# Performance work log

Measured on AMD Instinct MI355X. Metric: run time of the kernel, lower is better.

## Reference

```python
import jax, jax.numpy as jnp
import numpy as np

B, C, N, D, H, NC = 128, 9, 2048, 192, 384, 18  # batch, in_chans, time, embed, mlp_hidden, classes


def setup_inputs() -> dict:
    key = jax.random.key(0)
    ks = jax.random.split(key, 18)
    rn = lambda k, sh, s=0.02: jax.random.normal(k, sh, dtype=jnp.float32) * s
    return {
        "x": jax.random.normal(ks[0], (B, C, N), dtype=jnp.float32),
        "conv_w": rn(ks[1], (D, C, 3)),
        "conv_b": jnp.zeros((D,), jnp.float32),
        "pos_embed": jnp.zeros((1, N, D), jnp.float32),
        "qkv_w": rn(ks[2], (3 * D, D)),
        "qkv_b": jnp.zeros((3 * D,), jnp.float32),
        "proj_w": rn(ks[3], (D, D)),
        "proj_b": jnp.zeros((D,), jnp.float32),
        "ln1_g": jnp.ones((D,), jnp.float32),
        "ln1_b": jnp.zeros((D,), jnp.float32),
        "mlp_w1": rn(ks[4], (H, D)),
        "mlp_b1": jnp.zeros((H,), jnp.float32),
        "mlp_w2": rn(ks[5], (D, H)),
        "mlp_b2": jnp.zeros((D,), jnp.float32),
        "ln2_g": jnp.ones((D,), jnp.float32),
        "ln2_b": jnp.zeros((D,), jnp.float32),
        "head_w": rn(ks[6], (NC, D)),
        "head_b": jnp.zeros((NC,), jnp.float32),
    }


def _ln(x, g, b, eps=1e-5):
    m = x.mean(-1, keepdims=True)
    v = ((x - m) ** 2).mean(-1, keepdims=True)
    return (x - m) * jax.lax.rsqrt(v + eps) * g + b


def reference(x, conv_w, conv_b, pos_embed, qkv_w, qkv_b, proj_w, proj_b,
              ln1_g, ln1_b, mlp_w1, mlp_b1, mlp_w2, mlp_b2, ln2_g, ln2_b,
              head_w, head_b):
    # patch embed: Conv1d(C->D, k=3, pad=1), then [B, N, D]
    h = jax.lax.conv_general_dilated(
        x, conv_w, window_strides=(1,), padding=[(1, 1)],
        dimension_numbers=("NCH", "OIH", "NCH")) + conv_b[None, :, None]
    h = jnp.transpose(h, (0, 2, 1)) + pos_embed  # [B, N, D]

    # linear (Performer-style) attention with ReLU feature maps
    hn = _ln(h, ln1_g, ln1_b)
    qkv = hn @ qkv_w.T + qkv_b  # [B, N, 3D]
    q, k, v = jnp.split(qkv, 3, axis=-1)
    q = jax.nn.relu(q)
    k = jax.nn.relu(k)
    kv = jnp.einsum("bnd,bne->bde", k, v)       # [B, D, D]
    num = jnp.einsum("bnd,bde->bne", q, kv)      # [B, N, D]
    # NOTE: original sums q over BOTH token and feature dims -> scalar per batch
    denom = q.sum(axis=(1, 2))[:, None, None]
    attn = num / (denom + 1e-6)
    h = h + attn @ proj_w.T + proj_b

    # MLP block (exact GELU, as torch nn.GELU default)
    hn2 = _ln(h, ln2_g, ln2_b)
    m = jax.nn.gelu(hn2 @ mlp_w1.T + mlp_b1, approximate=False)
    h = h + m @ mlp_w2.T + mlp_b2

    # head: AdaptiveAvgPool1d(1) over time, then Linear
    pooled = h.mean(axis=1)  # [B, D]
    return pooled @ head_w.T + head_b  # [B, NC]
```

## Files before the change

kernel.cpp:

```cpp
#include <hip/hip_runtime.h>
#include <cmath>

#define B_   128
#define C_   9
#define N_   2048
#define D_   192
#define H_   384
#define NC_  18

typedef unsigned short ushort_t;
typedef __attribute__((ext_vector_type(8))) __bf16 bf16x8;
typedef __attribute__((ext_vector_type(8))) short short8;
typedef __attribute__((ext_vector_type(16))) float f32x16;

__device__ __forceinline__ ushort_t f2bf(float x) {
    unsigned u = __float_as_uint(x);
    return (ushort_t)((u + 0x7fffu + ((u >> 16) & 1u)) >> 16);
}
__device__ __forceinline__ float bf2f(ushort_t h) {
    return __uint_as_float(((unsigned)h) << 16);
}
__device__ __forceinline__ bf16x8 ldfrag(const ushort_t* p) {
    short8 s = *(const short8*)p;
    return __builtin_bit_cast(bf16x8, s);
}

#define APAD 12480

__global__ __launch_bounds__(192) void conv_ln_k(
    const float* __restrict__ x, const float* __restrict__ w,
    const float* __restrict__ cb, const float* __restrict__ pos,
    const float* __restrict__ lng, const float* __restrict__ lnb,
    float* __restrict__ h, ushort_t* __restrict__ oh, ushort_t* __restrict__ ol)
{
    const int n0 = blockIdx.x * 64;
    const int b  = blockIdx.y;
    const int d  = threadIdx.x;

    __shared__ float xs[C_][66];
    __shared__ float tile[64][193];
    __shared__ float ps[64][3], pq[64][3];
    __shared__ float mm[64], rr[64];

    for (int e = threadIdx.x; e < C_ * 66; e += 192) {
        int c = e / 66, i = e % 66;
        int n = n0 - 1 + i;
        xs[c][i] = (n >= 0 && n < N_) ? x[((size_t)b * C_ + c) * N_ + n] : 0.f;
    }
    float wr[C_][3];
#pragma unroll
    for (int c = 0; c < C_; ++c)
#pragma unroll
        for (int t = 0; t < 3; ++t) wr[c][t] = w[(d * C_ + c) * 3 + t];
    const float bias = cb[d];
    __syncthreads();

    for (int i = 0; i < 64; ++i) {
        float acc = bias + pos[(size_t)(n0 + i) * D_ + d];
#pragma unroll
        for (int c = 0; c < C_; ++c)
#pragma unroll
            for (int t = 0; t < 3; ++t) acc += xs[c][i + t] * wr[c][t];
        tile[i][d] = acc;
    }
    __syncthreads();

    {
        int row = threadIdx.x & 63, part = threadIdx.x >> 6;
        float s = 0.f, q = 0.f;
        const float* tr = &tile[row][part * 64];
#pragma unroll 8
        for (int j = 0; j < 64; ++j) { float v = tr[j]; s += v; q += v * v; }
        ps[row][part] = s; pq[row][part] = q;
    }
    __syncthreads();
    if (threadIdx.x < 64) {
        int r = threadIdx.x;
        float s = ps[r][0] + ps[r][1] + ps[r][2];
        float q = pq[r][0] + pq[r][1] + pq[r][2];
        float m = s * (1.f / D_);
        mm[r] = m;
        rr[r] = rsqrtf(q * (1.f / D_) - m * m + 1e-5f);
    }
    __syncthreads();
    {
        const float gd = lng[d], bd = lnb[d];
        for (int i = 0; i < 64; ++i) {
            float v = tile[i][d];
            size_t idx = ((size_t)b * N_ + n0 + i) * D_ + d;
            h[idx] = v;
            float nv = (v - mm[i]) * rr[i] * gd + bd;
            ushort_t hb = f2bf(nv);
            oh[idx] = hb;
            ol[idx] = f2bf(nv - bf2f(hb));
        }
    }
}

__global__ __launch_bounds__(256) void splitw_pack_k(
    const float* __restrict__ w, ushort_t* __restrict__ hi, ushort_t* __restrict__ lo,
    int NW, int K)
{
    int i = blockIdx.x * 256 + threadIdx.x;
    if (i >= NW * K) return;
    int row = i / K, k = i % K;
    int g = row / 192, c = row % 192;
    float v = w[i];
    ushort_t hb = f2bf(v);
    size_t o = (size_t)g * K * 192 + (size_t)(k >> 4) * 3072 + (size_t)c * 16 + (k & 15);
    hi[o] = hb;
    lo[o] = f2bf(v - bf2f(hb));
}

template <int EPI, int KT, int NBY>
__global__ __launch_bounds__(256) void mgemm(
    const ushort_t* __restrict__ Ah, const ushort_t* __restrict__ Al,
    const ushort_t* __restrict__ Wh, const ushort_t* __restrict__ Wl,
    const float* __restrict__ bias, float* __restrict__ dsum,
    const float* __restrict__ lng, const float* __restrict__ lnb,
    ushort_t* __restrict__ oh, ushort_t* __restrict__ ol,
    ushort_t* __restrict__ kTh, ushort_t* __restrict__ kTl,
    ushort_t* __restrict__ vTh, ushort_t* __restrict__ vTl,
    float* __restrict__ facc)
{
    extern __shared__ ushort_t smem[];
    constexpr int NS  = KT / 16;
    constexpr int APL = 12288;

    const int tid  = threadIdx.x;
    const int lane = tid & 63;
    const int l5   = lane >> 5;
    const int wid  = tid >> 6;
    const int wr = wid >> 1, wc = wid & 1;

    int bx, by;
    {
        int gmx = gridDim.x / NBY;
        int xx = blockIdx.x & 7, ii = blockIdx.x >> 3;
        by = ii % NBY;
        bx = xx * (gmx >> 3) + ii / NBY;
    }
    const int m0 = bx * 64;
    const int batch = m0 >> 11;

    size_t wbase = 0;
    if (EPI == 0) wbase = (size_t)by * 192 * KT;
    else if (EPI == 3) wbase = (size_t)batch * D_ * D_;
    const ushort_t* Whp = Wh + wbase;
    const ushort_t* Wlp = Wl + wbase;

    auto stageChunk = [&](int kr) {
#pragma unroll
        for (int i = 0; i < 12; ++i) {
            int c = wid + i * 4;
            int plane = c & 1, k8 = c >> 1;
            const ushort_t* ap = plane ? Al : Ah;
            const ushort_t* src = ap + (size_t)(m0 + lane) * KT + kr * 192 + k8 * 8;
            __builtin_amdgcn_global_load_lds(
                (const __attribute__((address_space(1))) void*)src,
                (__attribute__((address_space(3))) void*)(smem + plane * APL + k8 * 512),
                16, 0, 0);
        }
    };

    const int wcol = (wc * 96 + (lane & 31)) * 16 + l5 * 8;
    auto loadW = [&](int sg, bf16x8* w) {
#pragma unroll
        for (int tn = 0; tn < 3; ++tn) {
            size_t off = (size_t)sg * 3072 + wcol + tn * 512;
            w[tn * 2 + 0] = ldfrag(Whp + off);
            w[tn * 2 + 1] = ldfrag(Wlp + off);
        }
    };

    f32x16 acc[3] = {};
    const int arow = (wr * 32 + (lane & 31)) * 8;

    bf16x8 w0[6], w1[6], w2[6];
    loadW(0, w0);
    if (NS > 1) loadW(1, w1);
    if (NS > 2) loadW(2, w2);

#pragma unroll
    for (int s = 0; s < NS; ++s) {
        if ((s % 12) == 0) {
            if (s) __syncthreads();
            stageChunk(s / 12);
            __syncthreads();
        }
        bf16x8* wcur = (s % 3 == 0) ? w0 : ((s % 3 == 1) ? w1 : w2);
        int ao = ((s % 12) * 2 + l5) * 512 + arow;
        bf16x8 ah = ldfrag(smem + ao);
        bf16x8 al = ldfrag(smem + APL + ao);
#pragma unroll
        for (int tn = 0; tn < 3; ++tn) {
            acc[tn] = __builtin_amdgcn_mfma_f32_32x32x16_bf16(ah, wcur[tn * 2 + 0], acc[tn], 0, 0, 0);
            acc[tn] = __builtin_amdgcn_mfma_f32_32x32x16_bf16(ah, wcur[tn * 2 + 1], acc[tn], 0, 0, 0);
            acc[tn] = __builtin_amdgcn_mfma_f32_32x32x16_bf16(al, wcur[tn * 2 + 0], acc[tn], 0, 0, 0);
        }
        if (s + 3 < NS) loadW(s + 3, wcur);
    }

    const int cb = wc * 96 + (lane & 31);
    const int rb0 = m0 + wr * 32 + 4 * l5;
    const int rl0 = wr * 32 + 4 * l5;

    if (EPI == 0) {
        if (by == 0) {
            float qsum = 0.f;
            __syncthreads();
#pragma unroll
            for (int tn = 0; tn < 3; ++tn) {
                const int col = cb + tn * 32;
                const float bv = bias[col];
#pragma unroll
                for (int r = 0; r < 16; ++r) {
                    int rowl = rl0 + (r & 3) + 8 * (r >> 2);
                    float v = fmaxf(acc[tn][r] + bv, 0.f);
                    qsum += v;
                    ushort_t hb = f2bf(v);
                    smem[rowl * 192 + col] = hb;
                    smem[APL + rowl * 192 + col] = f2bf(v - bf2f(hb));
                }
            }
            __syncthreads();
            {
                size_t gb = (size_t)m0 * 192;
#pragma unroll
                for (int j = 0; j < 6; ++j) {
                    int idx = (tid * 6 + j) * 8;
                    *(uint4*)(oh + gb + idx) = *(const uint4*)&smem[idx];
                    *(uint4*)(ol + gb + idx) = *(const uint4*)&smem[APL + idx];
                }
            }
            float* red = (float*)(smem + 2 * APL);
            red[tid] = qsum;
            __syncthreads();
            for (int o = 128; o > 0; o >>= 1) {
                if (tid < o) red[tid] += red[tid + o];
                __syncthreads();
            }
            if (tid == 0) dsum[batch * 32 + ((m0 >> 6) & 31)] = red[0];
        } else {
            ushort_t* dsth = (by == 1) ? kTh : vTh;
            ushort_t* dstl = (by == 1) ? kTl : vTl;
            constexpr int STR = 72;
#pragma unroll
            for (int plane = 0; plane < 2; ++plane) {
                __syncthreads();
#pragma unroll
                for (int tn = 0; tn < 3; ++tn) {
                    const int col = cb + tn * 32;
                    const float bv = bias[by * 192 + col];
#pragma unroll
                    for (int r = 0; r < 16; ++r) {
                        int rowl = rl0 + (r & 3) + 8 * (r >> 2);
                        float v = acc[tn][r] + bv;
                        if (by == 1) v = fmaxf(v, 0.f);
                        ushort_t hb = f2bf(v);
                        smem[col * STR + rowl] = plane ? f2bf(v - bf2f(hb)) : hb;
                    }
                }
                __syncthreads();
                if (tid < 192) {
                    ushort_t* dst = plane ? dstl : dsth;
                    size_t gbase = ((size_t)batch * 192 + tid) * (size_t)N_ + (m0 & 2047);
#pragma unroll
                    for (int i2 = 0; i2 < 8; ++i2)
                        *(uint4*)(dst + gbase + i2 * 8) = *(const uint4*)&smem[tid * STR + i2 * 8];
                }
            }
        }
    } else if (EPI == 3) {
        float ds = 0.f;
        const float* dp = dsum + batch * 32;
#pragma unroll
        for (int j = 0; j < 32; ++j) ds += dp[j];
        const float s = 1.f / (ds + 1e-6f);
#pragma unroll
        for (int tn = 0; tn < 3; ++tn) {
            const int col = cb + tn * 32;
            const float bv = bias[col];
#pragma unroll
            for (int r = 0; r < 16; ++r) {
                int row = rb0 + (r & 3) + 8 * (r >> 2);
                float v = facc[(size_t)row * D_ + col] + acc[tn][r] * s + bv;
                facc[(size_t)row * D_ + col] = v;
                acc[tn][r] = v;
            }
        }
        __syncthreads();
        float* ls = (float*)(smem + 2 * APL);
        float* lq = ls + 128;
        float* lm = lq + 128;
        float* lr = lm + 64;
#pragma unroll
        for (int r = 0; r < 16; ++r) {
            float pv = acc[0][r] + acc[1][r] + acc[2][r];
            float qv = acc[0][r] * acc[0][r] + acc[1][r] * acc[1][r] + acc[2][r] * acc[2][r];
#pragma unroll
            for (int off = 1; off <= 16; off <<= 1) {
                pv += __shfl_xor(pv, off);
                qv += __shfl_xor(qv, off);
            }
            if ((lane & 31) == 0) {
                int rl = rl0 + (r & 3) + 8 * (r >> 2);
                ls[rl * 2 + wc] = pv;
                lq[rl * 2 + wc] = qv;
            }
        }
        __syncthreads();
        if (tid < 64) {
            float sv = ls[tid * 2] + ls[tid * 2 + 1];
            float qv = lq[tid * 2] + lq[tid * 2 + 1];
            float mv = sv * (1.f / D_);
            lm[tid] = mv;
            lr[tid] = rsqrtf(qv * (1.f / D_) - mv * mv + 1e-5f);
        }
        __syncthreads();
#pragma unroll
        for (int tn = 0; tn < 3; ++tn) {
            const int col = cb + tn * 32;
            const float gv = lng[col], bv2 = lnb[col];
#pragma unroll
            for (int r = 0; r < 16; ++r) {
                int rl = rl0 + (r & 3) + 8 * (r >> 2);
                float nv = (acc[tn][r] - lm[rl]) * lr[rl] * gv + bv2;
                ushort_t hb = f2bf(nv);
                smem[rl * 192 + col] = hb;
                smem[APL + rl * 192 + col] = f2bf(nv - bf2f(hb));
            }
        }
        __syncthreads();
        {
            size_t gb = (size_t)m0 * 192;
#pragma unroll
            for (int j = 0; j < 6; ++j) {
                int idx = (tid * 6 + j) * 8;
                *(uint4*)(oh + gb + idx) = *(const uint4*)&smem[idx];
                *(uint4*)(ol + gb + idx) = *(const uint4*)&smem[APL + idx];
            }
        }
    }
}

__global__ __launch_bounds__(256) void fused_mlp(
    const ushort_t* __restrict__ Ah, const ushort_t* __restrict__ Al,
    const ushort_t* __restrict__ W1h, const ushort_t* __restrict__ W1l,
    const ushort_t* __restrict__ W2h, const ushort_t* __restrict__ W2l,
    const float* __restrict__ b1, const float* __restrict__ b2,
    float* __restrict__ h, float* __restrict__ pooled)
{
    extern __shared__ ushort_t smem[];

    const int tid  = threadIdx.x;
    const int lane = tid & 63;
    const int l5   = lane >> 5;
    const int wid  = tid >> 6;
    const int wr = wid >> 1, wc = wid & 1;

    int bx;
    { int xx = blockIdx.x & 7, ii = blockIdx.x >> 3; bx = xx * (gridDim.x >> 3) + ii; }
    const int m0 = bx * 64;
    const int batch = m0 >> 11;

#pragma unroll
    for (int i = 0; i < 12; ++i) {
        int c = wid + i * 4;
        int plane = c & 1, kk = c >> 1;
        const ushort_t* ap = plane ? Al : Ah;
        const ushort_t* src = ap + (size_t)(m0 + lane) * 192 + kk * 8;
        __builtin_amdgcn_global_load_lds(
            (const __attribute__((address_space(1))) void*)src,
            (__attribute__((address_space(3))) void*)(smem + plane * APAD + kk * 520),
            16, 0, 0);
    }

    const int wcol = (wc * 96 + (lane & 31)) * 16 + l5 * 8;
    const int arow = (wr * 32 + (lane & 31)) * 8;

    auto loadWf = [&](const ushort_t* Wh, const ushort_t* Wl, int sg, bf16x8* w) {
#pragma unroll
        for (int tn = 0; tn < 3; ++tn) {
            size_t off = (size_t)sg * 3072 + wcol + tn * 512;
            w[tn * 2 + 0] = ldfrag(Wh + off);
            w[tn * 2 + 1] = ldfrag(Wl + off);
        }
    };

    bf16x8 w0[6], w1[6], w2[6];
    loadWf(W1h, W1l, 0, w0);
    loadWf(W1h, W1l, 1, w1);
    loadWf(W1h, W1l, 2, w2);
    __syncthreads();

    f32x16 accm[2][3] = {};
#pragma unroll
    for (int g = 0; g < 2; ++g) {
        const ushort_t* Wh = W1h + g * 36864;
        const ushort_t* Wl = W1l + g * 36864;
        if (g) { loadWf(Wh, Wl, 0, w0); loadWf(Wh, Wl, 1, w1); loadWf(Wh, Wl, 2, w2); }
#pragma unroll
        for (int s = 0; s < 12; ++s) {
            bf16x8* wcur = (s % 3 == 0) ? w0 : ((s % 3 == 1) ? w1 : w2);
            int ao = (s * 2 + l5) * 520 + arow;
            bf16x8 ah = ldfrag(smem + ao);
            bf16x8 al = ldfrag(smem + APAD + ao);
#pragma unroll
            for (int tn = 0; tn < 3; ++tn) {
                accm[g][tn] = __builtin_amdgcn_mfma_f32_32x32x16_bf16(ah, wcur[tn * 2 + 0], accm[g][tn], 0, 0, 0);
                accm[g][tn] = __builtin_amdgcn_mfma_f32_32x32x16_bf16(ah, wcur[tn * 2 + 1], accm[g][tn], 0, 0, 0);
                accm[g][tn] = __builtin_amdgcn_mfma_f32_32x32x16_bf16(al, wcur[tn * 2 + 0], accm[g][tn], 0, 0, 0);
            }
            if (s + 3 < 12) loadWf(Wh, Wl, s + 3, wcur);
        }
    }

    f32x16 acco[3] = {};
#pragma unroll
    for (int g = 0; g < 2; ++g) {
        __syncthreads();
#pragma unroll
        for (int tn = 0; tn < 3; ++tn) {
            const int cl = wc * 96 + tn * 32 + (lane & 31);
            const float bv = b1[g * 192 + cl];
#pragma unroll
            for (int r = 0; r < 16; ++r) {
                int rowl = wr * 32 + 4 * l5 + (r & 3) + 8 * (r >> 2);
                float v = accm[g][tn][r] + bv;
                float gv = 0.5f * v * (1.f + erff(v * 0.70710678118654752f));
                ushort_t hb = f2bf(gv);
                int ad = (cl >> 3) * 520 + rowl * 8 + (cl & 7);
                smem[ad] = hb;
                smem[APAD + ad] = f2bf(gv - bf2f(hb));
            }
        }
        __syncthreads();
        loadWf(W2h, W2l, g * 12 + 0, w0);
        loadWf(W2h, W2l, g * 12 + 1, w1);
        loadWf(W2h, W2l, g * 12 + 2, w2);
#pragma unroll
        for (int s = 0; s < 12; ++s) {
            bf16x8* wcur = (s % 3 == 0) ? w0 : ((s % 3 == 1) ? w1 : w2);
            int ao = (s * 2 + l5) * 520 + arow;
            bf16x8 ah = ldfrag(smem + ao);
            bf16x8 al = ldfrag(smem + APAD + ao);
#pragma unroll
            for (int tn = 0; tn < 3; ++tn) {
                acco[tn] = __builtin_amdgcn_mfma_f32_32x32x16_bf16(ah, wcur[tn * 2 + 0], acco[tn], 0, 0, 0);
                acco[tn] = __builtin_amdgcn_mfma_f32_32x32x16_bf16(ah, wcur[tn * 2 + 1], acco[tn], 0, 0, 0);
                acco[tn] = __builtin_amdgcn_mfma_f32_32x32x16_bf16(al, wcur[tn * 2 + 0], acco[tn], 0, 0, 0);
            }
            if (s + 3 < 12) loadWf(W2h, W2l, g * 12 + s + 3, wcur);
        }
    }

    const int cb = wc * 96 + (lane & 31);
    const int rb0 = m0 + wr * 32 + 4 * l5;
    float tsum[3] = {0.f, 0.f, 0.f};
#pragma unroll
    for (int tn = 0; tn < 3; ++tn) {
        const int col = cb + tn * 32;
        const float bv = b2[col];
#pragma unroll
        for (int r = 0; r < 16; ++r) {
            int row = rb0 + (r & 3) + 8 * (r >> 2);
            float v = h[(size_t)row * D_ + col] + acco[tn][r] + bv;
            h[(size_t)row * D_ + col] = v;
            tsum[tn] += v;
        }
    }
#pragma unroll
    for (int tn = 0; tn < 3; ++tn) {
        float t = tsum[tn];
        t += __shfl_xor(t, 32);
        if (l5 == 0) atomicAdd(&pooled[(size_t)batch * D_ + cb + tn * 32], t);
    }
}

__global__ __launch_bounds__(256) void mgemm_kv(
    const ushort_t* __restrict__ Ah, const ushort_t* __restrict__ Al,
    const ushort_t* __restrict__ Wh, const ushort_t* __restrict__ Wl,
    float* __restrict__ facc, size_t span)
{
    extern __shared__ ushort_t smem[];
    constexpr int BM = 64;
    constexpr int APL = BM * 32, AK = BM * 8, AELEMS = BM * 64;
    constexpr int BUFE = AELEMS + 12288;
    constexpr int ACH = 8, NCH = ACH + 24;

    const int tid  = threadIdx.x;
    const int lane = tid & 63;
    const int l5   = lane >> 5;
    const int wid  = tid >> 6;
    const int wr = wid >> 1, wc = wid & 1;
    const int bx = blockIdx.x;
    const int m0 = bx * BM;

    const size_t wbase = (size_t)(bx / 3) * 192 * (size_t)N_;
    const ushort_t* Whp = Wh + wbase;
    const ushort_t* Wlp = Wl + wbase;

    const int seg = N_ / gridDim.z;
    const int kbeg = blockIdx.z * seg, kend = kbeg + seg;

    auto stage = [&](int buf, int k0) {
        const int base = buf * BUFE;
#pragma unroll
        for (int i = 0; i < NCH / 4; ++i) {
            int c = wid + i * 4;
            const ushort_t* src;
            int dst;
            if (c < ACH) {
                int koct = c & 3, tt = c >> 2;
                int plane = tt & 1;
                const ushort_t* ap = plane ? Al : Ah;
                src = ap + (size_t)(m0 + lane) * N_ + k0 + koct * 8;
                dst = plane * APL + koct * AK;
            } else {
                int c2 = c - ACH;
                int koct = c2 & 3, tt = c2 >> 2;
                int plane = tt & 1, rb = tt >> 1;
                const ushort_t* wp = plane ? Wlp : Whp;
                src = wp + (size_t)(rb * 64 + lane) * N_ + k0 + koct * 8;
                dst = AELEMS + plane * 6144 + koct * 1536 + rb * 512;
            }
            __builtin_amdgcn_global_load_lds(
                (const __attribute__((address_space(1))) void*)src,
                (__attribute__((address_space(3))) void*)(smem + base + dst),
                16, 0, 0);
        }
    };

    f32x16 acc[3] = {};

    const int nt = (kend - kbeg) / 32;
    stage(0, kbeg);
    __syncthreads();
    int cur = 0;
    for (int t = 0; t < nt; ++t) {
        if (t + 1 < nt) stage(cur ^ 1, kbeg + (t + 1) * 32);
        const ushort_t* bb = smem + cur * BUFE;
#pragma unroll
        for (int kh = 0; kh < 2; ++kh) {
            int ao = (kh * 2 + l5) * AK + (wr * 32 + (lane & 31)) * 8;
            bf16x8 ah = ldfrag(bb + ao);
            bf16x8 al = ldfrag(bb + APL + ao);
#pragma unroll
            for (int tn = 0; tn < 3; ++tn) {
                int wo = AELEMS + (kh * 2 + l5) * 1536 + (wc * 96 + tn * 32 + (lane & 31)) * 8;
                bf16x8 wh = ldfrag(bb + wo);
                bf16x8 wl = ldfrag(bb + wo + 6144);
                acc[tn] = __builtin_amdgcn_mfma_f32_32x32x16_bf16(ah, wh, acc[tn], 0, 0, 0);
                acc[tn] = __builtin_amdgcn_mfma_f32_32x32x16_bf16(ah, wl, acc[tn], 0, 0, 0);
                acc[tn] = __builtin_amdgcn_mfma_f32_32x32x16_bf16(al, wh, acc[tn], 0, 0, 0);
            }
        }
        __syncthreads();
        cur ^= 1;
    }

    float* fz = facc + (size_t)blockIdx.z * span;
    const int cb = wc * 96 + (lane & 31);
    const int rb0 = m0 + wr * 32 + 4 * l5;
#pragma unroll
    for (int tn = 0; tn < 3; ++tn) {
        const int col = cb + tn * 32;
#pragma unroll
        for (int r = 0; r < 16; ++r) {
            int row = rb0 + (r & 3) + 8 * (r >> 2);
            fz[(size_t)row * D_ + col] = acc[tn][r];
        }
    }
}

__global__ __launch_bounds__(256) void kv2_k(
    const float* __restrict__ pw, const float* __restrict__ kvs, size_t span,
    ushort_t* __restrict__ oh, ushort_t* __restrict__ ol)
{
    __shared__ float As[16][68];
    __shared__ float Ws[16][68];
    const int tid = threadIdx.x;
    const int tx = tid & 15, ty = tid >> 4;
    const int m0 = blockIdx.x * 64;
    const int n0 = blockIdx.y * 64;
    const int b = blockIdx.z;
    const int lm = tid >> 2;
    const int lk = (tid & 3) * 4;

    float acc[4][4] = {};
    for (int k0 = 0; k0 < D_; k0 += 16) {
        float4 av = *(const float4*)(pw + (size_t)(m0 + lm) * D_ + k0 + lk);
        As[lk + 0][lm] = av.x; As[lk + 1][lm] = av.y;
        As[lk + 2][lm] = av.z; As[lk + 3][lm] = av.w;
        const float* base = kvs + (size_t)b * D_ * D_ + (size_t)(n0 + lm) * D_ + k0 + lk;
        float4 wv = {0.f, 0.f, 0.f, 0.f};
#pragma unroll
        for (int z = 0; z < 8; ++z) {
            float4 t = *(const float4*)(base + z * span);
            wv.x += t.x; wv.y += t.y; wv.z += t.z; wv.w += t.w;
        }
        Ws[lk + 0][lm] = wv.x; Ws[lk + 1][lm] = wv.y;
        Ws[lk + 2][lm] = wv.z; Ws[lk + 3][lm] = wv.w;
        __syncthreads();
#pragma unroll
        for (int kk = 0; kk < 16; ++kk) {
            float4 a4 = *(const float4*)&As[kk][ty * 4];
            float4 w4 = *(const float4*)&Ws[kk][tx * 4];
            float a[4] = {a4.x, a4.y, a4.z, a4.w};
            float w[4] = {w4.x, w4.y, w4.z, w4.w};
#pragma unroll
            for (int i = 0; i < 4; ++i)
#pragma unroll
                for (int j = 0; j < 4; ++j) acc[i][j] += a[i] * w[j];
        }
        __syncthreads();
    }
    const int d0 = n0 + tx * 4;
#pragma unroll
    for (int i = 0; i < 4; ++i) {
        ushort_t hb[4], lb[4];
#pragma unroll
        for (int j = 0; j < 4; ++j) {
            float v = acc[i][j];
            hb[j] = f2bf(v);
            lb[j] = f2bf(v - bf2f(hb[j]));
        }
        const int e = m0 + ty * 4 + i;
        size_t off = (size_t)b * D_ * D_ + ((size_t)(d0 >> 4) * 192 + e) * 16 + (d0 & 15);
        *(uint2*)&oh[off] = make_uint2((unsigned)hb[0] | ((unsigned)hb[1] << 16),
                                       (unsigned)hb[2] | ((unsigned)hb[3] << 16));
        *(uint2*)&ol[off] = make_uint2((unsigned)lb[0] | ((unsigned)lb[1] << 16),
                                       (unsigned)lb[2] | ((unsigned)lb[3] << 16));
    }
}

__global__ __launch_bounds__(192) void head_k(
    const float* __restrict__ pooled, const float* __restrict__ hw,
    const float* __restrict__ hb, float* __restrict__ out)
{
    const int b = blockIdx.x, d = threadIdx.x;
    __shared__ float p[D_];
    p[d] = pooled[(size_t)b * D_ + d] * (1.f / N_);
    __syncthreads();
    if (d < NC_) {
        float acc = hb[d];
        for (int e = 0; e < D_; ++e) acc += p[e] * hw[d * D_ + e];
        out[b * NC_ + d] = acc;
    }
}

extern "C" void kernel_launch(void* const* d_in, const int* in_sizes, int n_in,
                              void* d_out, int out_size, void* d_ws, size_t ws_size,
                              hipStream_t stream) {
    (void)in_sizes; (void)n_in; (void)out_size;

    const float* x      = (const float*)d_in[0];
    const float* conv_w = (const float*)d_in[1];
    const float* conv_b = (const float*)d_in[2];
    const float* pos    = (const float*)d_in[3];
    const float* qkv_w  = (const float*)d_in[4];
    const float* qkv_b  = (const float*)d_in[5];
    const float* proj_w = (const float*)d_in[6];
    const float* proj_b = (const float*)d_in[7];
    const float* ln1_g  = (const float*)d_in[8];
    const float* ln1_b  = (const float*)d_in[9];
    const float* mlp_w1 = (const float*)d_in[10];
    const float* mlp_b1 = (const float*)d_in[11];
    const float* mlp_w2 = (const float*)d_in[12];
    const float* mlp_b2 = (const float*)d_in[13];
    const float* ln2_g  = (const float*)d_in[14];
    const float* ln2_b  = (const float*)d_in[15];
    const float* head_w = (const float*)d_in[16];
    const float* head_b = (const float*)d_in[17];
    float* out = (float*)d_out;

    const size_t perB =
        (size_t)N_ * D_ * 4 +
        (size_t)N_ * D_ * 2 * 2 +
        (size_t)N_ * D_ * 2 * 2 +
        (size_t)N_ * D_ * 2 * 4 +
        (size_t)D_ * D_ * 2 * 2 +
        16384;
    const size_t fixedW = 2ull * (576 * 192 + 384 * 192 + 192 * 384) * 2 + 65536;
    int BC = B_;
    while (BC > 1 && fixedW + (size_t)BC * perB > ws_size) BC >>= 1;
    const int nchunks = B_ / BC;
    const size_t rows = (size_t)BC * N_;

    char* p = (char*)d_ws;
    auto alloc = [&](size_t bytes) -> char* {
        char* r = p;
        p += (bytes + 255) & ~(size_t)255;
        return r;
    };
    ushort_t* qw_hi = (ushort_t*)alloc(576 * 192 * 2);
    ushort_t* qw_lo = (ushort_t*)alloc(576 * 192 * 2);
    ushort_t* w1_hi = (ushort_t*)alloc(384 * 192 * 2);
    ushort_t* w1_lo = (ushort_t*)alloc(384 * 192 * 2);
    ushort_t* w2_hi = (ushort_t*)alloc(192 * 384 * 2);
    ushort_t* w2_lo = (ushort_t*)alloc(192 * 384 * 2);

    const size_t szPl = rows * D_ * 2;
    float*    h      = (float*)alloc(rows * D_ * 4);
    ushort_t* hn_hi  = (ushort_t*)alloc(szPl);
    ushort_t* hn_lo  = (ushort_t*)alloc(szPl);
    ushort_t* q_hi   = (ushort_t*)alloc(szPl);
    ushort_t* q_lo   = (ushort_t*)alloc(szPl);
    ushort_t* kT_hi  = (ushort_t*)alloc(szPl);
    ushort_t* kT_lo  = (ushort_t*)alloc(szPl);
    ushort_t* vT_hi  = (ushort_t*)alloc(szPl);
    ushort_t* vT_lo  = (ushort_t*)alloc(szPl);
    ushort_t* kv2t_h = (ushort_t*)alloc((size_t)BC * D_ * D_ * 2);
    ushort_t* kv2t_l = (ushort_t*)alloc((size_t)BC * D_ * D_ * 2);
    float*    dsum   = (float*)alloc((size_t)BC * 32 * 4);
    float*    pooled = (float*)alloc((size_t)BC * D_ * 4);
    ushort_t* m_hi   = kT_hi;
    ushort_t* m_lo   = vT_hi;
    (void)m_hi; (void)m_lo;
    float*    kvs    = (float*)hn_hi;
    const size_t kvspan = (size_t)BC * D_ * D_;

    splitw_pack_k<<<(576 * 192 + 255) / 256, 256, 0, stream>>>(qkv_w, qw_hi, qw_lo, 576, 192);
    splitw_pack_k<<<(384 * 192 + 255) / 256, 256, 0, stream>>>(mlp_w1, w1_hi, w1_lo, 384, 192);
    splitw_pack_k<<<(192 * 384 + 255) / 256, 256, 0, stream>>>(mlp_w2, w2_hi, w2_lo, 192, 384);

    const int gm = (int)(rows / 64);
    const size_t SHQ = 50688;
    const size_t SHM = (size_t)APAD * 2 * 2;
    const size_t SH4 = (size_t)(64 * 64 + 12288) * 2 * 2;

    for (int ch = 0; ch < nchunks; ++ch) {
        const int b0 = ch * BC;
        const float* xc = x + (size_t)b0 * C_ * N_;

        hipMemsetAsync(pooled, 0, (size_t)BC * D_ * 4, stream);

        conv_ln_k<<<dim3(N_ / 64, BC), 192, 0, stream>>>(
            xc, conv_w, conv_b, pos, ln1_g, ln1_b, h, hn_hi, hn_lo);
        mgemm<0, 192, 3><<<gm * 3, 256, SHQ, stream>>>(
            hn_hi, hn_lo, qw_hi, qw_lo, qkv_b, dsum, nullptr, nullptr,
            q_hi, q_lo, kT_hi, kT_lo, vT_hi, vT_lo, nullptr);
        mgemm_kv<<<dim3(BC * 3, 1, 8), 256, SH4, stream>>>(
            kT_hi, kT_lo, vT_hi, vT_lo, kvs, kvspan);
        kv2_k<<<dim3(3, 3, BC), 256, 0, stream>>>(proj_w, kvs, kvspan, kv2t_h, kv2t_l);
        mgemm<3, 192, 1><<<gm, 256, SHQ, stream>>>(
            q_hi, q_lo, kv2t_h, kv2t_l, proj_b, dsum, ln2_g, ln2_b,
            hn_hi, hn_lo, nullptr, nullptr, nullptr, nullptr, h);
        fused_mlp<<<gm, 256, SHM, stream>>>(
            hn_hi, hn_lo, w1_hi, w1_lo, w2_hi, w2_lo, mlp_b1, mlp_b2, h, pooled);
        head_k<<<BC, 192, 0, stream>>>(pooled, head_w, head_b, out + (size_t)b0 * NC_);
    }
}
```

Baseline: 1.584 ms.

## Split fused MLP across hidden halves with atomic accumulation; pool residual in proj epilogue

```diff
diff --git a/kernel.cpp b/kernel.cpp
--- a/kernel.cpp
+++ b/kernel.cpp
@@ -25,7 +25,8 @@
     return __builtin_bit_cast(bf16x8, s);
 }
 
-#define APAD 12480
+#define APL12 12288
+#define APAD  12480
 
 __global__ __launch_bounds__(192) void conv_ln_k(
     const float* __restrict__ x, const float* __restrict__ w,
@@ -121,11 +122,11 @@
     ushort_t* __restrict__ oh, ushort_t* __restrict__ ol,
     ushort_t* __restrict__ kTh, ushort_t* __restrict__ kTl,
     ushort_t* __restrict__ vTh, ushort_t* __restrict__ vTl,
-    float* __restrict__ facc)
+    float* __restrict__ facc, float* __restrict__ pooledp)
 {
     extern __shared__ ushort_t smem[];
     constexpr int NS  = KT / 16;
-    constexpr int APL = 12288;
+    constexpr int APL = APL12;
 
     const int tid  = threadIdx.x;
     const int lane = tid & 63;
@@ -277,6 +278,7 @@
 #pragma unroll
         for (int j = 0; j < 32; ++j) ds += dp[j];
         const float s = 1.f / (ds + 1e-6f);
+        float tsum[3] = {0.f, 0.f, 0.f};
 #pragma unroll
         for (int tn = 0; tn < 3; ++tn) {
             const int col = cb + tn * 32;
@@ -287,7 +289,14 @@
                 float v = facc[(size_t)row * D_ + col] + acc[tn][r] * s + bv;
                 facc[(size_t)row * D_ + col] = v;
                 acc[tn][r] = v;
-            }
+                tsum[tn] += v;
+            }
+        }
+#pragma unroll
+        for (int tn = 0; tn < 3; ++tn) {
+            float t = tsum[tn];
+            t += __shfl_xor(t, 32);
+            if (l5 == 0) atomicAdd(&pooledp[(size_t)batch * D_ + cb + tn * 32], t);
         }
         __syncthreads();
         float* ls = (float*)(smem + 2 * APL);
@@ -344,7 +353,7 @@
     }
 }
 
-__global__ __launch_bounds__(256) void fused_mlp(
+__global__ __launch_bounds__(256) void fused_mlp_g(
     const ushort_t* __restrict__ Ah, const ushort_t* __restrict__ Al,
     const ushort_t* __restrict__ W1h, const ushort_t* __restrict__ W1l,
     const ushort_t* __restrict__ W2h, const ushort_t* __restrict__ W2l,
@@ -359,20 +368,25 @@
     const int wid  = tid >> 6;
     const int wr = wid >> 1, wc = wid & 1;
 
-    int bx;
-    { int xx = blockIdx.x & 7, ii = blockIdx.x >> 3; bx = xx * (gridDim.x >> 3) + ii; }
+    int bx, g;
+    {
+        int gmx = gridDim.x / 2;
+        int xx = blockIdx.x & 7, ii = blockIdx.x >> 3;
+        g = ii & 1;
+        bx = xx * (gmx >> 3) + (ii >> 1);
+    }
     const int m0 = bx * 64;
     const int batch = m0 >> 11;
 
 #pragma unroll
     for (int i = 0; i < 12; ++i) {
         int c = wid + i * 4;
-        int plane = c & 1, kk = c >> 1;
+        int plane = c & 1, k8 = c >> 1;
         const ushort_t* ap = plane ? Al : Ah;
-        const ushort_t* src = ap + (size_t)(m0 + lane) * 192 + kk * 8;
+        const ushort_t* src = ap + (size_t)(m0 + lane) * 192 + k8 * 8;
         __builtin_amdgcn_global_load_lds(
             (const __attribute__((address_space(1))) void*)src,
-            (__attribute__((address_space(3))) void*)(smem + plane * APAD + kk * 520),
+            (__attribute__((address_space(3))) void*)(smem + plane * APAD + k8 * 520),
             16, 0, 0);
     }
 
@@ -388,87 +402,84 @@
         }
     };
 
+    const ushort_t* Wg1h = W1h + g * 36864;
+    const ushort_t* Wg1l = W1l + g * 36864;
+
     bf16x8 w0[6], w1[6], w2[6];
-    loadWf(W1h, W1l, 0, w0);
-    loadWf(W1h, W1l, 1, w1);
-    loadWf(W1h, W1l, 2, w2);
-    __syncthreads();
-
-    f32x16 accm[2][3] = {};
-#pragma unroll
-    for (int g = 0; g < 2; ++g) {
-        const ushort_t* Wh = W1h + g * 36864;
-        const ushort_t* Wl = W1l + g * 36864;
-        if (g) { loadWf(Wh, Wl, 0, w0); loadWf(Wh, Wl, 1, w1); loadWf(Wh, Wl, 2, w2); }
-#pragma unroll
-        for (int s = 0; s < 12; ++s) {
-            bf16x8* wcur = (s % 3 == 0) ? w0 : ((s % 3 == 1) ? w1 : w2);
-            int ao = (s * 2 + l5) * 520 + arow;
-            bf16x8 ah = ldfrag(smem + ao);
-            bf16x8 al = ldfrag(smem + APAD + ao);
-#pragma unroll
-            for (int tn = 0; tn < 3; ++tn) {
-                accm[g][tn] = __builtin_amdgcn_mfma_f32_32x32x16_bf16(ah, wcur[tn * 2 + 0], accm[g][tn], 0, 0, 0);
-                accm[g][tn] = __builtin_amdgcn_mfma_f32_32x32x16_bf16(ah, wcur[tn * 2 + 1], accm[g][tn], 0, 0, 0);
-                accm[g][tn] = __builtin_amdgcn_mfma_f32_32x32x16_bf16(al, wcur[tn * 2 + 0], accm[g][tn], 0, 0, 0);
-            }
-            if (s + 3 < 12) loadWf(Wh, Wl, s + 3, wcur);
-        }
-    }
+    loadWf(Wg1h, Wg1l, 0, w0);
+    loadWf(Wg1h, Wg1l, 1, w1);
+    loadWf(Wg1h, Wg1l, 2, w2);
+    __syncthreads();
+
+    f32x16 accm[3] = {};
+#pragma unroll
+    for (int s = 0; s < 12; ++s) {
+        bf16x8* wcur = (s % 3 == 0) ? w0 : ((s % 3 == 1) ? w1 : w2);
+        int ao = (s * 2 + l5) * 520 + arow;
+        bf16x8 ah = ldfrag(smem + ao);
+        bf16x8 al = ldfrag(smem + APAD + ao);
+#pragma unroll
+        for (int tn = 0; tn < 3; ++tn) {
+            accm[tn] = __builtin_amdgcn_mfma_f32_32x32x16_bf16(ah, wcur[tn * 2 + 0], accm[tn], 0, 0, 0);
+            accm[tn] = __builtin_amdgcn_mfma_f32_32x32x16_bf16(ah, wcur[tn * 2 + 1], accm[tn], 0, 0, 0);
+            accm[tn] = __builtin_amdgcn_mfma_f32_32x32x16_bf16(al, wcur[tn * 2 + 0], accm[tn], 0, 0, 0);
+        }
+        if (s + 3 < 12) loadWf(Wg1h, Wg1l, s + 3, wcur);
+    }
+
+    __syncthreads();
+#pragma unroll
+    for (int tn = 0; tn < 3; ++tn) {
+        const int cl = wc * 96 + tn * 32 + (lane & 31);
+        const float bv = b1[g * 192 + cl];
+#pragma unroll
+        for (int r = 0; r < 16; ++r) {
+            int rowl = wr * 32 + 4 * l5 + (r & 3) + 8 * (r >> 2);
+            float v = accm[tn][r] + bv;
+            float gv = 0.5f * v * (1.f + erff(v * 0.70710678118654752f));
+            ushort_t hb = f2bf(gv);
+            int ad = (cl >> 3) * 520 + rowl * 8 + (cl & 7);
+            smem[ad] = hb;
+            smem[APAD + ad] = f2bf(gv - bf2f(hb));
+        }
+    }
+    __syncthreads();
 
     f32x16 acco[3] = {};
-#pragma unroll
-    for (int g = 0; g < 2; ++g) {
-        __syncthreads();
+    loadWf(W2h, W2l, g * 12 + 0, w0);
+    loadWf(W2h, W2l, g * 12 + 1, w1);
+    loadWf(W2h, W2l, g * 12 + 2, w2);
+#pragma unroll
+    for (int s = 0; s < 12; ++s) {
+        bf16x8* wcur = (s % 3 == 0) ? w0 : ((s % 3 == 1) ? w1 : w2);
+        int ao = (s * 2 + l5) * 520 + arow;
+        bf16x8 ah = ldfrag(smem + ao);
+        bf16x8 al = ldfrag(smem + APAD + ao);
 #pragma unroll
         for (int tn = 0; tn < 3; ++tn) {
-            const int cl = wc * 96 + tn * 32 + (lane & 31);
-            const float bv = b1[g * 192 + cl];
-#pragma unroll
-            for (int r = 0; r < 16; ++r) {
-                int rowl = wr * 32 + 4 * l5 + (r & 3) + 8 * (r >> 2);
-                float v = accm[g][tn][r] + bv;
-                float gv = 0.5f * v * (1.f + erff(v * 0.70710678118654752f));
-                ushort_t hb = f2bf(gv);
-                int ad = (cl >> 3) * 520 + rowl * 8 + (cl & 7);
-                smem[ad] = hb;
-                smem[APAD + ad] = f2bf(gv - bf2f(hb));
-            }
-        }
-        __syncthreads();
-        loadWf(W2h, W2l, g * 12 + 0, w0);
-        loadWf(W2h, W2l, g * 12 + 1, w1);
-        loadWf(W2h, W2l, g * 12 + 2, w2);
-#pragma unroll
-        for (int s = 0; s < 12; ++s) {
-            bf16x8* wcur = (s % 3 == 0) ? w0 : ((s % 3 == 1) ? w1 : w2);
-            int ao = (s * 2 + l5) * 520 + arow;
-            bf16x8 ah = ldfrag(smem + ao);
-            bf16x8 al = ldfrag(smem + APAD + ao);
-#pragma unroll
-            for (int tn = 0; tn < 3; ++tn) {
-                acco[tn] = __builtin_amdgcn_mfma_f32_32x32x16_bf16(ah, wcur[tn * 2 + 0], acco[tn], 0, 0, 0);
-                acco[tn] = __builtin_amdgcn_mfma_f32_32x32x16_bf16(ah, wcur[tn * 2 + 1], acco[tn], 0, 0, 0);
-                acco[tn] = __builtin_amdgcn_mfma_f32_32x32x16_bf16(al, wcur[tn * 2 + 0], acco[tn], 0, 0, 0);
-            }
-            if (s + 3 < 12) loadWf(W2h, W2l, g * 12 + s + 3, wcur);
-        }
+            acco[tn] = __builtin_amdgcn_mfma_f32_32x32x16_bf16(ah, wcur[tn * 2 + 0], acco[tn], 0, 0, 0);
+            acco[tn] = __builtin_amdgcn_mfma_f32_32x32x16_bf16(ah, wcur[tn * 2 + 1], acco[tn], 0, 0, 0);
+            acco[tn] = __builtin_amdgcn_mfma_f32_32x32x16_bf16(al, wcur[tn * 2 + 0], acco[tn], 0, 0, 0);
+        }
+        if (s + 3 < 12) loadWf(W2h, W2l, g * 12 + s + 3, wcur);
     }
 
     const int cb = wc * 96 + (lane & 31);
     const int rb0 = m0 + wr * 32 + 4 * l5;
-    float tsum[3] = {0.f, 0.f, 0.f};
+    float tsum[3];
 #pragma unroll
     for (int tn = 0; tn < 3; ++tn) {
         const int col = cb + tn * 32;
-        const float bv = b2[col];
+        const float bv = (g == 0) ? b2[col] : 0.f;
+        float t = 16.f * bv;
 #pragma unroll
         for (int r = 0; r < 16; ++r) {
             int row = rb0 + (r & 3) + 8 * (r >> 2);
-            float v = h[(size_t)row * D_ + col] + acco[tn][r] + bv;
-            h[(size_t)row * D_ + col] = v;
-            tsum[tn] += v;
-        }
+            float pv = acco[tn][r] + bv;
+            atomicAdd(&h[(size_t)row * D_ + col], pv);
+            t += acco[tn][r];
+        }
+        tsum[tn] = t;
     }
 #pragma unroll
     for (int tn = 0; tn < 3; ++tn) {
@@ -715,9 +726,6 @@
     ushort_t* kv2t_l = (ushort_t*)alloc((size_t)BC * D_ * D_ * 2);
     float*    dsum   = (float*)alloc((size_t)BC * 32 * 4);
     float*    pooled = (float*)alloc((size_t)BC * D_ * 4);
-    ushort_t* m_hi   = kT_hi;
-    ushort_t* m_lo   = vT_hi;
-    (void)m_hi; (void)m_lo;
     float*    kvs    = (float*)hn_hi;
     const size_t kvspan = (size_t)BC * D_ * D_;
 
@@ -727,7 +735,7 @@
 
     const int gm = (int)(rows / 64);
     const size_t SHQ = 50688;
-    const size_t SHM = (size_t)APAD * 2 * 2;
+    const size_t SHG = (size_t)APAD * 2 * 2;
     const size_t SH4 = (size_t)(64 * 64 + 12288) * 2 * 2;
 
     for (int ch = 0; ch < nchunks; ++ch) {
@@ -740,14 +748,14 @@
             xc, conv_w, conv_b, pos, ln1_g, ln1_b, h, hn_hi, hn_lo);
         mgemm<0, 192, 3><<<gm * 3, 256, SHQ, stream>>>(
             hn_hi, hn_lo, qw_hi, qw_lo, qkv_b, dsum, nullptr, nullptr,
-            q_hi, q_lo, kT_hi, kT_lo, vT_hi, vT_lo, nullptr);
+            q_hi, q_lo, kT_hi, kT_lo, vT_hi, vT_lo, nullptr, nullptr);
         mgemm_kv<<<dim3(BC * 3, 1, 8), 256, SH4, stream>>>(
             kT_hi, kT_lo, vT_hi, vT_lo, kvs, kvspan);
         kv2_k<<<dim3(3, 3, BC), 256, 0, stream>>>(proj_w, kvs, kvspan, kv2t_h, kv2t_l);
         mgemm<3, 192, 1><<<gm, 256, SHQ, stream>>>(
             q_hi, q_lo, kv2t_h, kv2t_l, proj_b, dsum, ln2_g, ln2_b,
-            hn_hi, hn_lo, nullptr, nullptr, nullptr, nullptr, h);
-        fused_mlp<<<gm, 256, SHM, stream>>>(
+            hn_hi, hn_lo, nullptr, nullptr, nullptr, nullptr, h, pooled);
+        fused_mlp_g<<<gm * 2, 256, SHG, stream>>>(
             hn_hi, hn_lo, w1_hi, w1_lo, w2_hi, w2_lo, mlp_b1, mlp_b2, h, pooled);
         head_k<<<BC, 192, 0, stream>>>(pooled, head_w, head_b, out + (size_t)b0 * NC_);
     }
```

Result: slower. 1.708 ms (+7.9%).
